# Optimization experiments

Measured on AMD Instinct MI355X. Metric: run time of the kernel, lower is better.

The kernel has to match this reference:

```python
import jax, jax.numpy as jnp
import numpy as np

ALPHA = 0.2  # LeakyReLU negative slope
NEG_INF = -9e15


def setup_inputs() -> dict:
    key = jax.random.key(0)
    k1, k2, k3, k4 = jax.random.split(key, 4)
    B, N, F_in, F_out = 8, 2048, 256, 128
    x = jax.random.normal(k1, (B, N, F_in), dtype=jnp.float32)
    adj = jax.random.randint(k2, (B, N, N), 0, 2, dtype=jnp.int32)
    # xavier-uniform-like init
    limW = float(np.sqrt(6.0 / (F_in + F_out)))
    W = jax.random.uniform(k3, (F_in, F_out), jnp.float32, -limW, limW)
    lima = float(np.sqrt(6.0 / (2 * F_out + 1)))
    a = jax.random.uniform(k4, (2 * F_out, 1), jnp.float32, -lima, lima)
    return {"x": x, "adj": adj, "W": W, "a": a}


def reference(x, adj, W, a):
    # x: [B, N, F_in], adj: [B, N, N], W: [F_in, F_out], a: [2*F_out, 1]
    F_out = W.shape[1]
    h = jnp.einsum('bnf,fo->bno', x, W)            # [B, N, F_out]
    a1 = a[:F_out, 0]                               # attends to source node i
    a2 = a[F_out:, 0]                               # attends to target node j
    f1 = h @ a1                                     # [B, N]
    f2 = h @ a2                                     # [B, N]
    # e[b,i,j] = leakyrelu(a1.h_i + a2.h_j) -- factored form of the concat trick
    e = jax.nn.leaky_relu(f1[:, :, None] + f2[:, None, :], negative_slope=ALPHA)
    attention = jnp.where(adj > 0, e, NEG_INF)
    attention = jax.nn.softmax(attention, axis=2)   # [B, N, N]
    # dropout is identity in eval mode
    h_prime = jnp.einsum('bij,bjo->bio', attention, h)  # [B, N, F_out]
    return jax.nn.elu(h_prime)                      # concat=True -> ELU
```

## Files before the change

### kernel.cpp

```cpp
#include <hip/hip_runtime.h>
#include <stdint.h>

#define BB   8
#define NN   2048
#define FIN  256
#define FOUT 128

using short8 = __attribute__((ext_vector_type(8))) short;
using f32x4  = __attribute__((ext_vector_type(4))) float;

__device__ __forceinline__ unsigned short rbf(float f) {
    return (unsigned short)((__float_as_uint(f) + 0x8000u) >> 16);
}

__device__ __forceinline__ void mfma_calib(int m, int quad, int* Mlab, int* Nlab) {
    short8 pa1, pb1, pa2, pb2;
    const short one = (short)0x3F80;
    const short mb  = (short)rbf((float)m);
#pragma unroll
    for (int j = 0; j < 8; ++j) { pa1[j] = 0; pa2[j] = 0; pb1[j] = mb; pb2[j] = one; }
    if (quad == 0) { pa1[0] = one; pa2[0] = mb; }
    f32x4 zz = {0.f, 0.f, 0.f, 0.f};
    f32x4 c1 = __builtin_amdgcn_mfma_f32_16x16x32_bf16(pa1, pb1, zz, 0, 0, 0);
    f32x4 c2 = __builtin_amdgcn_mfma_f32_16x16x32_bf16(pa2, pb2, zz, 0, 0, 0);
#pragma unroll
    for (int r = 0; r < 4; ++r) {
        Nlab[r] = ((int)c1[r]) & 15;
        Mlab[r] = ((int)c2[r]) & 15;
    }
}

__global__ __launch_bounds__(256) void gat_wt(const float* __restrict__ W,
                                              unsigned short* __restrict__ wt) {
    const int g  = blockIdx.x * 256 + threadIdx.x;
    const int k  = g >> 5;
    const int o4 = (g & 31) << 2;
    float4 wv = *(const float4*)(W + (k << 7) + o4);
    wt[((o4 + 0) << 8) + k] = rbf(wv.x);
    wt[((o4 + 1) << 8) + k] = rbf(wv.y);
    wt[((o4 + 2) << 8) + k] = rbf(wv.z);
    wt[((o4 + 3) << 8) + k] = rbf(wv.w);
}

__global__ __launch_bounds__(256) void gat_h3(
        const float* __restrict__ x, const unsigned short* __restrict__ wt,
        const float* __restrict__ a, unsigned short* __restrict__ ht,
        float* __restrict__ f1, float* __restrict__ f2) {
    __shared__ unsigned short xs[16][264];
    __shared__ float hs[16][132];
    const int bk   = blockIdx.x;
    const int R0   = bk << 4;
    const int b    = R0 >> 11;
    const int il0  = R0 & (NN - 1);
    const int tid  = threadIdx.x;
    const int w    = tid >> 6;
    const int lane = tid & 63;
    const int m    = lane & 15;
    const int quad = lane >> 4;

#pragma unroll
    for (int rr = 0; rr < 4; ++rr) {
        const int row = (w << 2) + rr;
        float4 xv = *(const float4*)(x + (size_t)(R0 + row) * FIN + (lane << 2));
        ushort4 c4;
        c4.x = rbf(xv.x); c4.y = rbf(xv.y); c4.z = rbf(xv.z); c4.w = rbf(xv.w);
        *(ushort4*)(&xs[row][lane << 2]) = c4;
    }
    int Mlab[4], Nlab[4];
    mfma_calib(m, quad, Mlab, Nlab);
    __syncthreads();

    f32x4 zz = {0.f, 0.f, 0.f, 0.f};
    f32x4 acc[2] = {zz, zz};
#pragma unroll
    for (int kc = 0; kc < 8; ++kc) {
        const int k0 = (kc << 5) + (quad << 3);
        short8 av = *(const short8*)(&xs[m][k0]);
#pragma unroll
        for (int t = 0; t < 2; ++t) {
            const int ot = (w << 1) + t;
            short8 bw = *(const short8*)(wt + (((ot << 4) + m) << 8) + k0);
            acc[t] = __builtin_amdgcn_mfma_f32_16x16x32_bf16(av, bw, acc[t], 0, 0, 0);
        }
    }
#pragma unroll
    for (int t = 0; t < 2; ++t)
#pragma unroll
        for (int r = 0; r < 4; ++r)
            hs[Mlab[r]][(((w << 1) + t) << 4) + Nlab[r]] = acc[t][r];
    __syncthreads();

    {
        const int i   = tid >> 4;
        const int seg = tid & 15;
        const int o0  = seg << 3;
        float s1 = 0.f, s2 = 0.f;
#pragma unroll
        for (int e = 0; e < 8; ++e) {
            float hv = hs[i][o0 + e];
            s1 = fmaf(hv, a[o0 + e], s1);
            s2 = fmaf(hv, a[FOUT + o0 + e], s2);
        }
        s1 += __shfl_xor(s1, 1); s1 += __shfl_xor(s1, 2);
        s1 += __shfl_xor(s1, 4); s1 += __shfl_xor(s1, 8);
        s2 += __shfl_xor(s2, 1); s2 += __shfl_xor(s2, 2);
        s2 += __shfl_xor(s2, 4); s2 += __shfl_xor(s2, 8);
        if (seg == 0) { f1[R0 + i] = s1; f2[R0 + i] = s2; }
    }
    {
        const int o  = tid >> 1;
        const int i8 = (tid & 1) << 3;
        short8 hv;
#pragma unroll
        for (int e = 0; e < 8; ++e) hv[e] = (short)rbf(hs[i8 + e][o]);
        *(short8*)(ht + ((size_t)((b << 7) + o) << 11) + il0 + i8) = hv;
    }
}

__global__ __launch_bounds__(256, 1) void gat_s5(
        const int* __restrict__ adj, const unsigned short* __restrict__ ht,
        const float* __restrict__ f1, const float* __restrict__ f2,
        float* __restrict__ out) {
    const int bk   = blockIdx.x;
    const int b    = bk & 7;
    const int i0   = (bk >> 3) << 6;
    const int tid  = threadIdx.x;
    const int w    = tid >> 6;
    const int lane = tid & 63;
    const int m    = lane & 15;
    const int quad = lane >> 4;

    __shared__ float accb[64][132];
    __shared__ float sbuf[4][4][16];

    int Mlab[4], Nlab[4];
    mfma_calib(m, quad, Mlab, Nlab);

    const int gi0 = (b << 11) + i0;
    float f1v[4];
    const int* adjr[4];
#pragma unroll
    for (int g = 0; g < 4; ++g) {
        f1v[g]  = f1[gi0 + (g << 4) + m];
        adjr[g] = adj + ((size_t)(gi0 + (g << 4) + m) << 11);
    }
    const float* f2b = f2 + (b << 11);
    const unsigned short* htb = ht + ((size_t)b << 18);

    f32x4 zz = {0.f, 0.f, 0.f, 0.f};
    f32x4 acc[4][8];
#pragma unroll
    for (int g = 0; g < 4; ++g)
#pragma unroll
        for (int t = 0; t < 8; ++t) acc[g][t] = zz;
    float sp[4] = {0.f, 0.f, 0.f, 0.f};

    const int jb = (w << 9) + (quad << 3);
    for (int c = 0; c < 16; ++c) {
        const int j0 = jb + (c << 5);
        short8 hf[8];
#pragma unroll
        for (int ot = 0; ot < 8; ++ot)
            hf[ot] = *(const short8*)(htb + ((size_t)((ot << 4) + m) << 11) + j0);

        float4 fa = *(const float4*)(f2b + j0);
        float4 fb = *(const float4*)(f2b + j0 + 4);
        float fm[8] = {fa.x, fa.y, fa.z, fa.w, fb.x, fb.y, fb.z, fb.w};

#pragma unroll
        for (int g = 0; g < 4; ++g) {
            int4 a0 = *(const int4*)(adjr[g] + j0);
            int4 a1 = *(const int4*)(adjr[g] + j0 + 4);
            int am[8] = {a0.x, a0.y, a0.z, a0.w, a1.x, a1.y, a1.z, a1.w};
            const float f1r = f1v[g];
            float p[8];
#pragma unroll
            for (int u = 0; u < 8; ++u) {
                float e = f1r + fm[u];
                p[u] = (am[u] > 0) ? __expf(fmaxf(e, 0.2f * e)) : 0.f;
            }
            sp[g] += ((p[0] + p[1]) + (p[2] + p[3])) + ((p[4] + p[5]) + (p[6] + p[7]));
            short8 pf;
#pragma unroll
            for (int u = 0; u < 8; ++u) pf[u] = (short)rbf(p[u]);
#pragma unroll
            for (int ot = 0; ot < 8; ++ot)
                acc[g][ot] = __builtin_amdgcn_mfma_f32_16x16x32_bf16(pf, hf[ot], acc[g][ot], 0, 0, 0);
        }
    }

#pragma unroll
    for (int g = 0; g < 4; ++g) {
        float v = sp[g];
        v += __shfl_xor(v, 16); v += __shfl_xor(v, 32);
        if (lane < 16) sbuf[w][g][lane] = v;
    }

#pragma unroll
    for (int p = 0; p < 4; ++p) {
        const int g = (w + p) & 3;
        if (p == 0) {
#pragma unroll
            for (int ot = 0; ot < 8; ++ot)
#pragma unroll
                for (int r = 0; r < 4; ++r)
                    accb[(g << 4) + Mlab[r]][(ot << 4) + Nlab[r]] = acc[g][ot][r];
        } else {
#pragma unroll
            for (int ot = 0; ot < 8; ++ot)
#pragma unroll
                for (int r = 0; r < 4; ++r)
                    accb[(g << 4) + Mlab[r]][(ot << 4) + Nlab[r]] += acc[g][ot][r];
        }
        __syncthreads();
    }

    {
        const int row = tid >> 2;
        const int o0  = (tid & 3) << 5;
        const int g   = row >> 4;
        const int mm  = row & 15;
        const float s = (sbuf[0][g][mm] + sbuf[1][g][mm]) +
                        (sbuf[2][g][mm] + sbuf[3][g][mm]);
        const float inv = 1.0f / s;
        float* orow = out + (((size_t)gi0 + row) << 7) + o0;
#pragma unroll
        for (int v4 = 0; v4 < 8; ++v4) {
            float4 rv;
            float y;
            y = accb[row][o0 + 4 * v4 + 0] * inv; rv.x = y > 0.f ? y : expm1f(y);
            y = accb[row][o0 + 4 * v4 + 1] * inv; rv.y = y > 0.f ? y : expm1f(y);
            y = accb[row][o0 + 4 * v4 + 2] * inv; rv.z = y > 0.f ? y : expm1f(y);
            y = accb[row][o0 + 4 * v4 + 3] * inv; rv.w = y > 0.f ? y : expm1f(y);
            *(float4*)(orow + 4 * v4) = rv;
        }
    }
}

extern "C" void kernel_launch(void* const* d_in, const int* in_sizes, int n_in,
                              void* d_out, int out_size, void* d_ws, size_t ws_size,
                              hipStream_t stream) {
    const float* x   = nullptr;
    const int*   adj = nullptr;
    const float* W   = nullptr;
    const float* a   = nullptr;
    for (int i = 0; i < n_in; ++i) {
        const long s = in_sizes[i];
        if      (s == (long)BB * NN * NN)  adj = (const int*)d_in[i];
        else if (s == (long)BB * NN * FIN) x   = (const float*)d_in[i];
        else if (s == (long)FIN * FOUT)    W   = (const float*)d_in[i];
        else if (s == 2L * FOUT)           a   = (const float*)d_in[i];
    }
    if (!x)   x   = (const float*)d_in[0];
    if (!adj) adj = (const int*)d_in[1];
    if (!W)   W   = (const float*)d_in[2];
    if (!a)   a   = (const float*)d_in[3];
    float* out = (float*)d_out;

    unsigned short* wt = (unsigned short*)d_ws;
    unsigned short* ht = wt + 32768;
    float* f1 = (float*)(ht + (size_t)BB * NN * FOUT);
    float* f2 = f1 + BB * NN;

    hipLaunchKernelGGL(gat_wt, dim3(32),   dim3(256), 0, stream, W, wt);
    hipLaunchKernelGGL(gat_h3, dim3(1024), dim3(256), 0, stream, x, wt, a, ht, f1, f2);
    hipLaunchKernelGGL(gat_s5, dim3(256),  dim3(256), 0, stream, adj, ht, f1, f2, out);
}
```

Before: 274.6 us.

## Pack adjacency into bitmask and split attention kernel over output-feature quarters

A new pre-pass kernel packs the int32 adjacency matrix into a 1-bit-per-edge mask with wavefront ballots. The attention kernel then reads mask words instead of int4 adjacency vectors, and its grid doubles by splitting the 128 output features into four 32-wide slices. Each block now covers 128 rows and runs with launch bounds allowing two blocks per CU. This raises occupancy and cuts the adjacency bytes read inside the main loop, at the cost of an extra full pass over adj and recomputing the exp/softmax weights four times, once per feature slice.

```diff
diff --git a/kernel.cpp b/kernel.cpp
--- a/kernel.cpp
+++ b/kernel.cpp
@@ -117,121 +117,136 @@
     }
 }
 
-__global__ __launch_bounds__(256, 1) void gat_s5(
-        const int* __restrict__ adj, const unsigned short* __restrict__ ht,
+__global__ __launch_bounds__(256) void gat_pk(const int* __restrict__ adj,
+                                              unsigned int* __restrict__ mask) {
+    const int w    = threadIdx.x >> 6;
+    const int lane = threadIdx.x & 63;
+    const size_t row = (size_t)blockIdx.x * 4 + w;
+    const int* ar = adj + (row << 11);
+    unsigned long long* mrow = (unsigned long long*)(mask + (row << 6));
+#pragma unroll 4
+    for (int k = 0; k < 32; ++k) {
+        int v = ar[(k << 6) + lane];
+        unsigned long long bm = __ballot(v > 0);
+        if (lane == 0) mrow[k] = bm;
+    }
+}
+
+__global__ __launch_bounds__(256, 2) void gat_s6(
+        const unsigned int* __restrict__ mask, const unsigned short* __restrict__ ht,
         const float* __restrict__ f1, const float* __restrict__ f2,
         float* __restrict__ out) {
     const int bk   = blockIdx.x;
     const int b    = bk & 7;
-    const int i0   = (bk >> 3) << 6;
+    const int it   = (bk >> 3) & 15;
+    const int oq   = bk >> 7;
+    const int i0   = it << 7;
+    const int ob   = oq << 5;
     const int tid  = threadIdx.x;
     const int w    = tid >> 6;
     const int lane = tid & 63;
     const int m    = lane & 15;
     const int quad = lane >> 4;
 
-    __shared__ float accb[64][132];
-    __shared__ float sbuf[4][4][16];
+    __shared__ float accb[128][33];
+    __shared__ float sbuf[4][8][16];
 
     int Mlab[4], Nlab[4];
     mfma_calib(m, quad, Mlab, Nlab);
 
     const int gi0 = (b << 11) + i0;
-    float f1v[4];
-    const int* adjr[4];
-#pragma unroll
-    for (int g = 0; g < 4; ++g) {
-        f1v[g]  = f1[gi0 + (g << 4) + m];
-        adjr[g] = adj + ((size_t)(gi0 + (g << 4) + m) << 11);
-    }
+    float f1v[8];
+#pragma unroll
+    for (int t = 0; t < 8; ++t) f1v[t] = f1[gi0 + (t << 4) + m];
+    const unsigned int* mbase = mask + (((size_t)(gi0 + m)) << 6) + (w << 4);
     const float* f2b = f2 + (b << 11);
-    const unsigned short* htb = ht + ((size_t)b << 18);
+    const unsigned short* ht0 = ht + ((size_t)b << 18) + ((size_t)(ob + m) << 11);
+    const unsigned short* ht1 = ht0 + (16 << 11);
 
     f32x4 zz = {0.f, 0.f, 0.f, 0.f};
-    f32x4 acc[4][8];
-#pragma unroll
-    for (int g = 0; g < 4; ++g)
-#pragma unroll
-        for (int t = 0; t < 8; ++t) acc[g][t] = zz;
-    float sp[4] = {0.f, 0.f, 0.f, 0.f};
+    f32x4 acc[8][2];
+#pragma unroll
+    for (int t = 0; t < 8; ++t) { acc[t][0] = zz; acc[t][1] = zz; }
+    float sp[8] = {0.f, 0.f, 0.f, 0.f, 0.f, 0.f, 0.f, 0.f};
 
     const int jb = (w << 9) + (quad << 3);
+    const int sh = quad << 3;
+#pragma unroll 2
     for (int c = 0; c < 16; ++c) {
         const int j0 = jb + (c << 5);
-        short8 hf[8];
-#pragma unroll
-        for (int ot = 0; ot < 8; ++ot)
-            hf[ot] = *(const short8*)(htb + ((size_t)((ot << 4) + m) << 11) + j0);
-
+        short8 hf0 = *(const short8*)(ht0 + j0);
+        short8 hf1 = *(const short8*)(ht1 + j0);
         float4 fa = *(const float4*)(f2b + j0);
         float4 fb = *(const float4*)(f2b + j0 + 4);
         float fm[8] = {fa.x, fa.y, fa.z, fa.w, fb.x, fb.y, fb.z, fb.w};
 
 #pragma unroll
-        for (int g = 0; g < 4; ++g) {
-            int4 a0 = *(const int4*)(adjr[g] + j0);
-            int4 a1 = *(const int4*)(adjr[g] + j0 + 4);
-            int am[8] = {a0.x, a0.y, a0.z, a0.w, a1.x, a1.y, a1.z, a1.w};
-            const float f1r = f1v[g];
+        for (int t = 0; t < 8; ++t) {
+            const unsigned int mw = mbase[(t << 10) + c];
+            const float f1r = f1v[t];
             float p[8];
 #pragma unroll
             for (int u = 0; u < 8; ++u) {
                 float e = f1r + fm[u];
-                p[u] = (am[u] > 0) ? __expf(fmaxf(e, 0.2f * e)) : 0.f;
+                float lr = fmaxf(e, 0.2f * e);
+                p[u] = ((mw >> (sh + u)) & 1u) ? __expf(lr) : 0.f;
             }
-            sp[g] += ((p[0] + p[1]) + (p[2] + p[3])) + ((p[4] + p[5]) + (p[6] + p[7]));
+            sp[t] += ((p[0] + p[1]) + (p[2] + p[3])) + ((p[4] + p[5]) + (p[6] + p[7]));
             short8 pf;
 #pragma unroll
             for (int u = 0; u < 8; ++u) pf[u] = (short)rbf(p[u]);
-#pragma unroll
-            for (int ot = 0; ot < 8; ++ot)
-                acc[g][ot] = __builtin_amdgcn_mfma_f32_16x16x32_bf16(pf, hf[ot], acc[g][ot], 0, 0, 0);
-        }
-    }
-
-#pragma unroll
-    for (int g = 0; g < 4; ++g) {
-        float v = sp[g];
+            acc[t][0] = __builtin_amdgcn_mfma_f32_16x16x32_bf16(pf, hf0, acc[t][0], 0, 0, 0);
+            acc[t][1] = __builtin_amdgcn_mfma_f32_16x16x32_bf16(pf, hf1, acc[t][1], 0, 0, 0);
+        }
+    }
+
+#pragma unroll
+    for (int t = 0; t < 8; ++t) {
+        float v = sp[t];
         v += __shfl_xor(v, 16); v += __shfl_xor(v, 32);
-        if (lane < 16) sbuf[w][g][lane] = v;
+        if (lane < 16) sbuf[w][t][lane] = v;
     }
 
 #pragma unroll
     for (int p = 0; p < 4; ++p) {
         const int g = (w + p) & 3;
-        if (p == 0) {
-#pragma unroll
-            for (int ot = 0; ot < 8; ++ot)
-#pragma unroll
-                for (int r = 0; r < 4; ++r)
-                    accb[(g << 4) + Mlab[r]][(ot << 4) + Nlab[r]] = acc[g][ot][r];
-        } else {
-#pragma unroll
-            for (int ot = 0; ot < 8; ++ot)
-#pragma unroll
-                for (int r = 0; r < 4; ++r)
-                    accb[(g << 4) + Mlab[r]][(ot << 4) + Nlab[r]] += acc[g][ot][r];
+#pragma unroll
+        for (int tt = 0; tt < 2; ++tt) {
+            const int t = (g << 1) + tt;
+            if (p == 0) {
+#pragma unroll
+                for (int r = 0; r < 4; ++r) {
+                    accb[(t << 4) + Mlab[r]][Nlab[r]]      = acc[t][0][r];
+                    accb[(t << 4) + Mlab[r]][16 + Nlab[r]] = acc[t][1][r];
+                }
+            } else {
+#pragma unroll
+                for (int r = 0; r < 4; ++r) {
+                    accb[(t << 4) + Mlab[r]][Nlab[r]]      += acc[t][0][r];
+                    accb[(t << 4) + Mlab[r]][16 + Nlab[r]] += acc[t][1][r];
+                }
+            }
         }
         __syncthreads();
     }
 
     {
-        const int row = tid >> 2;
-        const int o0  = (tid & 3) << 5;
-        const int g   = row >> 4;
+        const int row = tid >> 1;
+        const int ol  = (tid & 1) << 4;
+        const int t   = row >> 4;
         const int mm  = row & 15;
-        const float s = (sbuf[0][g][mm] + sbuf[1][g][mm]) +
-                        (sbuf[2][g][mm] + sbuf[3][g][mm]);
+        const float s = (sbuf[0][t][mm] + sbuf[1][t][mm]) +
+                        (sbuf[2][t][mm] + sbuf[3][t][mm]);
         const float inv = 1.0f / s;
-        float* orow = out + (((size_t)gi0 + row) << 7) + o0;
-#pragma unroll
-        for (int v4 = 0; v4 < 8; ++v4) {
+        float* orow = out + (((size_t)gi0 + row) << 7) + ob + ol;
+#pragma unroll
+        for (int v4 = 0; v4 < 4; ++v4) {
             float4 rv;
             float y;
-            y = accb[row][o0 + 4 * v4 + 0] * inv; rv.x = y > 0.f ? y : expm1f(y);
-            y = accb[row][o0 + 4 * v4 + 1] * inv; rv.y = y > 0.f ? y : expm1f(y);
-            y = accb[row][o0 + 4 * v4 + 2] * inv; rv.z = y > 0.f ? y : expm1f(y);
-            y = accb[row][o0 + 4 * v4 + 3] * inv; rv.w = y > 0.f ? y : expm1f(y);
+            y = accb[row][ol + 4 * v4 + 0] * inv; rv.x = y > 0.f ? y : expm1f(y);
+            y = accb[row][ol + 4 * v4 + 1] * inv; rv.y = y > 0.f ? y : expm1f(y);
+            y = accb[row][ol + 4 * v4 + 2] * inv; rv.z = y > 0.f ? y : expm1f(y);
+            y = accb[row][ol + 4 * v4 + 3] * inv; rv.w = y > 0.f ? y : expm1f(y);
             *(float4*)(orow + 4 * v4) = rv;
         }
     }
@@ -261,8 +276,10 @@
     unsigned short* ht = wt + 32768;
     float* f1 = (float*)(ht + (size_t)BB * NN * FOUT);
     float* f2 = f1 + BB * NN;
+    unsigned int* mask = (unsigned int*)(f2 + BB * NN);
 
     hipLaunchKernelGGL(gat_wt, dim3(32),   dim3(256), 0, stream, W, wt);
+    hipLaunchKernelGGL(gat_pk, dim3(4096), dim3(256), 0, stream, adj, mask);
     hipLaunchKernelGGL(gat_h3, dim3(1024), dim3(256), 0, stream, x, wt, a, ht, f1, f2);
-    hipLaunchKernelGGL(gat_s5, dim3(256),  dim3(256), 0, stream, adj, ht, f1, f2, out);
-}
+    hipLaunchKernelGGL(gat_s6, dim3(512),  dim3(256), 0, stream, mask, ht, f1, f2, out);
+}
```

New measurement: 295.4 us. 1.08x slower.
